# Performance work log

Hardware: AMD Instinct MI355X
Metric: run time of the kernel (lower is better)

Reference implementation:

```python
import jax, jax.numpy as jnp
import numpy as np

N = 100000   # nodes
E = 1600000  # message edges (avg degree 16)
L = 500000   # supervision (label) edges
IN = 128     # input feature dim
H = 2        # attention heads
C = 64       # hidden_dim per head
HC = H * C   # 128, per-layer output channels
DEC = 64     # decoder_dim
NEG_SLOPE = 0.2


def setup_inputs():
    key = jax.random.key(0)
    ks = jax.random.split(key, 16)
    s = 0.05
    return {
        "x": jax.random.normal(ks[0], (N, IN), jnp.float32),
        "edge_index": jax.random.randint(ks[1], (2, E), 0, N, dtype=jnp.int64),
        "edge_label_index": jax.random.randint(ks[2], (2, L), 0, N, dtype=jnp.int64),
        "W1": jax.random.normal(ks[3], (IN, HC), jnp.float32) * s,
        "att_src1": jax.random.normal(ks[4], (H, C), jnp.float32) * s,
        "att_dst1": jax.random.normal(ks[5], (H, C), jnp.float32) * s,
        "bias1": jnp.zeros((HC,), jnp.float32),
        "W2": jax.random.normal(ks[6], (HC, HC), jnp.float32) * s,
        "att_src2": jax.random.normal(ks[7], (H, C), jnp.float32) * s,
        "att_dst2": jax.random.normal(ks[8], (H, C), jnp.float32) * s,
        "bias2": jnp.zeros((HC,), jnp.float32),
        "lin1_w": jax.random.normal(ks[9], (2 * HC, DEC), jnp.float32) * s,
        "lin1_b": jnp.zeros((DEC,), jnp.float32),
        "lin2_w": jax.random.normal(ks[10], (DEC, 1), jnp.float32) * s,
        "lin2_b": jnp.zeros((1,), jnp.float32),
    }


def _gat_conv(x, src, dst, W, att_src, att_dst, bias, n_nodes):
    # PyG GATConv (concat=True, negative_slope=0.2), self-loops already in src/dst.
    h = (x @ W).reshape(-1, H, C)                       # [N, H, C]
    a_s = jnp.sum(h * att_src[None], axis=-1)           # [N, H]
    a_d = jnp.sum(h * att_dst[None], axis=-1)           # [N, H]
    e = jax.nn.leaky_relu(a_s[src] + a_d[dst], NEG_SLOPE)  # [E, H]
    m = jax.ops.segment_max(e, dst, num_segments=n_nodes)  # segment-softmax (stable)
    ex = jnp.exp(e - jax.lax.stop_gradient(m)[dst])
    denom = jax.ops.segment_sum(ex, dst, num_segments=n_nodes)
    alpha = ex / denom[dst]                             # [E, H]
    out = jax.ops.segment_sum(h[src] * alpha[:, :, None], dst, num_segments=n_nodes)
    return out.reshape(n_nodes, HC) + bias


def reference(x, edge_index, edge_label_index, W1, att_src1, att_dst1, bias1,
              W2, att_src2, att_dst2, bias2, lin1_w, lin1_b, lin2_w, lin2_b):
    n = x.shape[0]
    loop = jnp.arange(n, dtype=edge_index.dtype)
    src = jnp.concatenate([edge_index[0], loop])
    dst = jnp.concatenate([edge_index[1], loop])
    # encode (eval mode: dropout is a no-op)
    h1 = jax.nn.relu(_gat_conv(x, src, dst, W1, att_src1, att_dst1, bias1, n))
    z = _gat_conv(h1, src, dst, W2, att_src2, att_dst2, bias2, n)
    # decode
    hs = jnp.concatenate([z[edge_label_index[0]], z[edge_label_index[1]]], axis=1)
    hdec = jax.nn.relu(hs @ lin1_w + lin1_b)
    return (hdec @ lin2_w + lin2_b).reshape(-1)
```

## Files before the change

### kernel.cpp

```cpp
#include <hip/hip_runtime.h>
#include <hip/hip_fp16.h>


typedef _Float16 f16x8 __attribute__((ext_vector_type(8)));
typedef float f32x4 __attribute__((ext_vector_type(4)));

__device__ __forceinline__ float rl_f(float v, int lane) {
    return __int_as_float(__builtin_amdgcn_readlane(__float_as_int(v), lane));
}

#define WT_LD 136
__global__ __launch_bounds__(256, 3) void gemm_mfma(
    const float* __restrict__ X, const float* __restrict__ W,
    _Float16* __restrict__ Y, int nrows,
    const float* __restrict__ att_s, const float* __restrict__ att_d,
    float2* __restrict__ as_out, float2* __restrict__ ad_out)
{
    __shared__ _Float16 WT[128 * WT_LD];
    __shared__ _Float16 At[64 * WT_LD];
    const int t = threadIdx.x;
    const int lane = t & 63;
    const int wid = t >> 6;

    for (int i = t; i < 128 * 32; i += 256) {
        const int k = i >> 5;
        const int n4 = (i & 31) * 4;
        const float4 wv = *reinterpret_cast<const float4*>(&W[k * 128 + n4]);
        WT[(n4 + 0) * WT_LD + k] = (_Float16)wv.x;
        WT[(n4 + 1) * WT_LD + k] = (_Float16)wv.y;
        WT[(n4 + 2) * WT_LD + k] = (_Float16)wv.z;
        WT[(n4 + 3) * WT_LD + k] = (_Float16)wv.w;
    }

    const int am = lane & 15, ag = lane >> 4;

    float asv[8], adv[8];
    if (as_out) {
#pragma unroll
        for (int n0 = 0; n0 < 8; ++n0) {
            asv[n0] = att_s[n0 * 16 + am];
            adv[n0] = att_d[n0 * 16 + am];
        }
    }

    const int ntiles = (nrows + 63) >> 6;
    for (int tile = blockIdx.x; tile < ntiles; tile += gridDim.x) {
        const int rbase = tile * 64;
        __syncthreads();
        {
            const int r = t >> 2;
            const int c0 = (t & 3) * 32;
            const int gr = rbase + r;
            _Float16 tmp[32];
            if (gr < nrows) {
                const float* src = X + (size_t)gr * 128 + c0;
#pragma unroll
                for (int q = 0; q < 8; ++q) {
                    const float4 v = *reinterpret_cast<const float4*>(src + q * 4);
                    tmp[q * 4 + 0] = (_Float16)v.x; tmp[q * 4 + 1] = (_Float16)v.y;
                    tmp[q * 4 + 2] = (_Float16)v.z; tmp[q * 4 + 3] = (_Float16)v.w;
                }
            } else {
#pragma unroll
                for (int q = 0; q < 32; ++q) tmp[q] = (_Float16)0.f;
            }
#pragma unroll
            for (int q = 0; q < 4; ++q)
                *reinterpret_cast<f16x8*>(&At[r * WT_LD + c0 + q * 8]) =
                    *reinterpret_cast<const f16x8*>(&tmp[q * 8]);
        }
        __syncthreads();

        const int srow = wid * 16;
        f16x8 a[4];
#pragma unroll
        for (int kb = 0; kb < 4; ++kb)
            a[kb] = *reinterpret_cast<const f16x8*>(
                &At[(srow + am) * WT_LD + kb * 32 + ag * 8]);

        f32x4 acc[8];
#pragma unroll
        for (int n0 = 0; n0 < 8; ++n0) {
            f32x4 c = {0.f, 0.f, 0.f, 0.f};
#pragma unroll
            for (int kb = 0; kb < 4; ++kb) {
                const f16x8 b = *reinterpret_cast<const f16x8*>(
                    &WT[(n0 * 16 + am) * WT_LD + kb * 32 + ag * 8]);
                c = __builtin_amdgcn_mfma_f32_16x16x32_f16(a[kb], b, c, 0, 0, 0);
            }
            acc[n0] = c;
        }

        const int growbase = rbase + srow + ag * 4;

#pragma unroll
        for (int j = 0; j < 4; ++j) {
            const int grow = growbase + j;
            if (grow < nrows) {
#pragma unroll
                for (int n0 = 0; n0 < 8; ++n0)
                    Y[(size_t)grow * 128 + n0 * 16 + am] = (_Float16)acc[n0][j];
            }
        }

        if (as_out) {
#pragma unroll
            for (int j = 0; j < 4; ++j) {
                float s0 = 0.f, s1 = 0.f, d0 = 0.f, d1 = 0.f;
#pragma unroll
                for (int n0 = 0; n0 < 4; ++n0) {
                    s0 = fmaf(acc[n0][j], asv[n0], s0);
                    d0 = fmaf(acc[n0][j], adv[n0], d0);
                }
#pragma unroll
                for (int n0 = 4; n0 < 8; ++n0) {
                    s1 = fmaf(acc[n0][j], asv[n0], s1);
                    d1 = fmaf(acc[n0][j], adv[n0], d1);
                }
#pragma unroll
                for (int off = 1; off < 16; off <<= 1) {
                    s0 += __shfl_xor(s0, off, 64); s1 += __shfl_xor(s1, off, 64);
                    d0 += __shfl_xor(d0, off, 64); d1 += __shfl_xor(d1, off, 64);
                }
                const int grow = growbase + j;
                if (am == 0 && grow < nrows) {
                    as_out[grow] = make_float2(s0, s1);
                    ad_out[grow] = make_float2(d0, d1);
                }
            }
        }
    }
}

__global__ __launch_bounds__(256) void init_counts_k(int* __restrict__ counts, int N)
{
    const int i = blockIdx.x * blockDim.x + threadIdx.x;
    if (i < N) counts[i] = 1;
}

__global__ __launch_bounds__(256) void hist_k(
    const int* __restrict__ edst, int E, int* __restrict__ counts)
{
    const int stride = gridDim.x * blockDim.x;
    for (int e = blockIdx.x * blockDim.x + threadIdx.x; e < E; e += stride)
        atomicAdd(&counts[edst[e]], 1);
}

__global__ __launch_bounds__(256) void scan_phase1(
    const int* __restrict__ counts, int* __restrict__ blockSums, int N)
{
    __shared__ int wsum[4];
    const int b = blockIdx.x, t = threadIdx.x;
    const int base = b * 1024 + t * 4;
    int s = 0;
    if (base + 3 < N) {
        const int4 c = *reinterpret_cast<const int4*>(&counts[base]);
        s = c.x + c.y + c.z + c.w;
    } else {
#pragma unroll
        for (int k = 0; k < 4; ++k) if (base + k < N) s += counts[base + k];
    }
#pragma unroll
    for (int off = 32; off; off >>= 1) s += __shfl_xor(s, off, 64);
    if ((t & 63) == 0) wsum[t >> 6] = s;
    __syncthreads();
    if (t == 0) blockSums[b] = wsum[0] + wsum[1] + wsum[2] + wsum[3];
}

__global__ __launch_bounds__(256) void scan_phase2(
    int* __restrict__ blockSums, int nb, int* __restrict__ row_ptr, int N)
{
    __shared__ int wsum[4];
    __shared__ int carry_sh;
    const int t = threadIdx.x;
    if (t == 0) carry_sh = 0;
    __syncthreads();
    for (int base = 0; base < nb; base += 256) {
        const int i = base + t;
        const int v = (i < nb) ? blockSums[i] : 0;
        int x = v;
#pragma unroll
        for (int off = 1; off < 64; off <<= 1) {
            const int y = __shfl_up(x, off, 64);
            if ((t & 63) >= off) x += y;
        }
        if ((t & 63) == 63) wsum[t >> 6] = x;
        __syncthreads();
        int woff = 0;
        for (int w = 0; w < (t >> 6); ++w) woff += wsum[w];
        const int carry = carry_sh;
        if (i < nb) blockSums[i] = carry + woff + x - v;
        __syncthreads();
        if (t == 255) carry_sh = carry + woff + x;
        __syncthreads();
    }
    if (t == 0) row_ptr[N] = carry_sh;
}

__global__ __launch_bounds__(256) void scan_phase3(
    const int* __restrict__ counts, const int* __restrict__ blockSums,
    int* __restrict__ row_ptr, int N)
{
    __shared__ int wsum[4];
    const int b = blockIdx.x, t = threadIdx.x;
    const int base = b * 1024 + t * 4;
    int v0 = 0, v1 = 0, v2 = 0, v3 = 0;
    if (base + 3 < N) {
        const int4 c = *reinterpret_cast<const int4*>(&counts[base]);
        v0 = c.x; v1 = c.y; v2 = c.z; v3 = c.w;
    } else {
        if (base + 0 < N) v0 = counts[base + 0];
        if (base + 1 < N) v1 = counts[base + 1];
        if (base + 2 < N) v2 = counts[base + 2];
        if (base + 3 < N) v3 = counts[base + 3];
    }
    const int tsum = v0 + v1 + v2 + v3;
    int x = tsum;
#pragma unroll
    for (int off = 1; off < 64; off <<= 1) {
        const int y = __shfl_up(x, off, 64);
        if ((t & 63) >= off) x += y;
    }
    if ((t & 63) == 63) wsum[t >> 6] = x;
    __syncthreads();
    int woff = 0;
    for (int w = 0; w < (t >> 6); ++w) woff += wsum[w];
    int excl = blockSums[b] + woff + x - tsum;
    if (base + 0 < N) row_ptr[base + 0] = excl;
    if (base + 1 < N) row_ptr[base + 1] = excl + v0;
    if (base + 2 < N) row_ptr[base + 2] = excl + v0 + v1;
    if (base + 3 < N) row_ptr[base + 3] = excl + v0 + v1 + v2;
}

__global__ __launch_bounds__(256) void init_cursor_k(
    const int* __restrict__ row_ptr, int* __restrict__ cursor,
    int* __restrict__ csr_src, int N)
{
    const int i = blockIdx.x * blockDim.x + threadIdx.x;
    if (i < N) {
        const int p = row_ptr[i];
        csr_src[p] = i;
        cursor[i] = p + 1;
    }
}

__global__ __launch_bounds__(256) void scatter_xcd_k(
    const int* __restrict__ esrc, const int* __restrict__ edst, int E,
    int* __restrict__ cursor, int* __restrict__ csr_src, int npp)
{
    const int part = blockIdx.x & 7;
    const int lo = part * npp;
    const int hiN = lo + npp;
    const int bi = blockIdx.x >> 3;
    const int stride = (gridDim.x >> 3) * blockDim.x;
    for (int e = bi * blockDim.x + threadIdx.x; e < E; e += stride) {
        const int d = edst[e];
        if (d >= lo && d < hiN) {
            const int pos = atomicAdd(&cursor[d], 1);
            csr_src[pos] = esrc[e];
        }
    }
}

__global__ __launch_bounds__(256) void csr_aggregate(
    const int* __restrict__ row_ptr, const int* __restrict__ csr_src,
    const __half2* __restrict__ h2, const float2* __restrict__ as_,
    const float2* __restrict__ ad_, const float* __restrict__ bias,
    float* __restrict__ out, int N, int do_relu)
{
    const int lane = threadIdx.x & 63;
    const int node = (blockIdx.x * blockDim.x + threadIdx.x) >> 6;
    if (node >= N) return;

    const int start = row_ptr[node];
    const int end   = row_ptr[node + 1];
    const float2 ad = ad_[node];
    const bool hi = lane >= 32;

    float den0 = 0.f, den1 = 0.f;
    float accx = 0.f, accy = 0.f;

    for (int base = start; base < end; base += 64) {
        const int cnt = min(64, end - base);
        float ex0 = 0.f, ex1 = 0.f;
        int s = 0;
        if (lane < cnt) {
            s = csr_src[base + lane];
            const float2 as = as_[s];
            float e0 = as.x + ad.x; e0 = fmaxf(e0, 0.2f * e0);
            float e1 = as.y + ad.y; e1 = fmaxf(e1, 0.2f * e1);
            ex0 = __expf(e0); ex1 = __expf(e1);
            den0 += ex0; den1 += ex1;
        }
        int j = 0;
        for (; j + 8 <= cnt; j += 8) {
            unsigned idx[8];
            float ej[8];
            float2 hv[8];
#pragma unroll
            for (int q = 0; q < 8; ++q) {
                idx[q] = (unsigned)(__builtin_amdgcn_readlane(s, j + q) * 64 + lane);
                ej[q] = hi ? rl_f(ex1, j + q) : rl_f(ex0, j + q);
            }
#pragma unroll
            for (int q = 0; q < 8; ++q)
                hv[q] = __half22float2(h2[idx[q]]);
#pragma unroll
            for (int q = 0; q < 8; ++q) {
                accx = fmaf(ej[q], hv[q].x, accx);
                accy = fmaf(ej[q], hv[q].y, accy);
            }
        }
        for (; j < cnt; ++j) {
            const unsigned idx = (unsigned)(__builtin_amdgcn_readlane(s, j) * 64 + lane);
            const float e = hi ? rl_f(ex1, j) : rl_f(ex0, j);
            const float2 hv = __half22float2(h2[idx]);
            accx = fmaf(e, hv.x, accx);
            accy = fmaf(e, hv.y, accy);
        }
    }

#pragma unroll
    for (int off = 32; off; off >>= 1) {
        den0 += __shfl_xor(den0, off, 64);
        den1 += __shfl_xor(den1, off, 64);
    }
    const float rd = 1.f / (hi ? den1 : den0);
    const float2 bv = ((const float2*)bias)[lane];
    float vx = fmaf(accx, rd, bv.x);
    float vy = fmaf(accy, rd, bv.y);
    if (do_relu) { vx = fmaxf(vx, 0.f); vy = fmaxf(vy, 0.f); }
    ((float2*)out)[(size_t)node * 64 + lane] = make_float2(vx, vy);
}

__global__ void build_wuv(const float* __restrict__ lin1_w, float* __restrict__ Wuv)
{
    const int i = blockIdx.x * blockDim.x + threadIdx.x;
    if (i >= 128 * 128) return;
    const int k = i >> 7, j = i & 127;
    Wuv[i] = (j < 64) ? lin1_w[k * 64 + j] : lin1_w[(128 + k) * 64 + (j - 64)];
}

__global__ __launch_bounds__(256) void decode_k(
    const int* __restrict__ eli, int L_, const __half* __restrict__ uv,
    const float* __restrict__ lin1_b, const float* __restrict__ lin2_w,
    const float* __restrict__ lin2_b, float* __restrict__ out)
{
    const int lane = threadIdx.x & 63;
    const int wstride = (gridDim.x * blockDim.x) >> 6;
    for (int wid = (blockIdx.x * blockDim.x + threadIdx.x) >> 6; wid < L_; wid += wstride) {
        const int a = eli[wid], b = eli[L_ + wid];
        const unsigned ia = (unsigned)(a * 128 + lane);
        const unsigned ib = (unsigned)(b * 128 + 64 + lane);
        float x = __half2float(uv[ia]) + __half2float(uv[ib]) + lin1_b[lane];
        x = x > 0.f ? x : 0.f;
        float p = x * lin2_w[lane];
#pragma unroll
        for (int off = 32; off; off >>= 1) p += __shfl_xor(p, off, 64);
        if (lane == 0) out[wid] = p + lin2_b[0];
    }
}

extern "C" void kernel_launch(void* const* d_in, const int* in_sizes, int n_in,
                              void* d_out, int out_size, void* d_ws, size_t ws_size,
                              hipStream_t stream)
{
    const float* x     = (const float*)d_in[0];
    const int*   ei    = (const int*)d_in[1];
    const int*   eli   = (const int*)d_in[2];
    const float* W1    = (const float*)d_in[3];
    const float* atts1 = (const float*)d_in[4];
    const float* attd1 = (const float*)d_in[5];
    const float* bias1 = (const float*)d_in[6];
    const float* W2    = (const float*)d_in[7];
    const float* atts2 = (const float*)d_in[8];
    const float* attd2 = (const float*)d_in[9];
    const float* bias2 = (const float*)d_in[10];
    const float* lin1w = (const float*)d_in[11];
    const float* lin1b = (const float*)d_in[12];
    const float* lin2w = (const float*)d_in[13];
    const float* lin2b = (const float*)d_in[14];
    float* out = (float*)d_out;

    const int N = in_sizes[0] / 128;
    const int E = in_sizes[1] / 2;
    const int L = in_sizes[2] / 2;

    float* ws   = (float*)d_ws;
    __half2* h16 = (__half2*)ws;
    float* x2z  = ws + (size_t)N * 64;
    float* a_s  = x2z + (size_t)N * 128;
    float* a_d  = a_s + (size_t)N * 2;
    float* Wuv  = a_d + (size_t)N * 2;
    int* row_ptr = (int*)(Wuv + 128 * 128);
    int* counts  = row_ptr + (N + 4);
    int* cursor  = counts + N;
    int* csr_src = cursor + N;
    int* blockSums = csr_src + (E + N);

    const int nBlocks256 = (N + 255) / 256;
    const int nb = (N + 1023) / 1024;
    const int npp = (N + 7) / 8;
    const int ntiles = (N + 63) / 64;
    const int gemmGrid = ntiles < 768 ? ntiles : 768;

    init_counts_k<<<nBlocks256, 256, 0, stream>>>(counts, N);
    hist_k<<<2048, 256, 0, stream>>>(ei + E, E, counts);
    scan_phase1<<<nb, 256, 0, stream>>>(counts, blockSums, N);
    scan_phase2<<<1, 256, 0, stream>>>(blockSums, nb, row_ptr, N);
    scan_phase3<<<nb, 256, 0, stream>>>(counts, blockSums, row_ptr, N);
    init_cursor_k<<<nBlocks256, 256, 0, stream>>>(row_ptr, cursor, csr_src, N);
    scatter_xcd_k<<<2048, 256, 0, stream>>>(ei, ei + E, E, cursor, csr_src, npp);

    for (int layer = 0; layer < 2; ++layer) {
        const float* xin  = (layer == 0) ? x : x2z;
        const float* W    = (layer == 0) ? W1 : W2;
        const float* as_w = (layer == 0) ? atts1 : atts2;
        const float* ad_w = (layer == 0) ? attd1 : attd2;
        const float* bs   = (layer == 0) ? bias1 : bias2;

        gemm_mfma<<<gemmGrid, 256, 0, stream>>>(xin, W, (_Float16*)h16, N, as_w, ad_w,
                                                (float2*)a_s, (float2*)a_d);
        csr_aggregate<<<(N + 3) / 4, 256, 0, stream>>>(row_ptr, csr_src, h16,
                                                       (const float2*)a_s, (const float2*)a_d,
                                                       bs, x2z, N, (layer == 0) ? 1 : 0);
    }

    build_wuv<<<64, 256, 0, stream>>>(lin1w, Wuv);
    gemm_mfma<<<gemmGrid, 256, 0, stream>>>(x2z, Wuv, (_Float16*)h16, N,
                                            nullptr, nullptr, nullptr, nullptr);
    decode_k<<<8192, 256, 0, stream>>>(eli, L, (const __half*)h16, lin1b, lin2w, lin2b, out);
}
```

Before: 459.3 us.

## Use mixed-precision FMA for half gathers and XCD-partition the degree histogram

The aggregation and decode kernels now use inline v_fma_mix_f32 so packed fp16 values feed the FMA directly, dropping the separate half-to-float conversions. The degree histogram is split into eight destination partitions keyed on block index, matching the existing scatter kernel, so each partition's atomics land on one XCD's L2. Decode also hoists its per-lane bias and weight loads out of the edge loop. Partitioning means every block reads all edges and filters them, which adds read traffic in exchange for more local atomics, and the inline asm ties the code to gfx9-class ISA.

```diff
diff --git a/kernel.cpp b/kernel.cpp
--- a/kernel.cpp
+++ b/kernel.cpp
@@ -7,6 +7,15 @@
 
 __device__ __forceinline__ float rl_f(float v, int lane) {
     return __int_as_float(__builtin_amdgcn_readlane(__float_as_int(v), lane));
+}
+
+__device__ __forceinline__ void fma_mix_lo(float& acc, unsigned hv, float e) {
+    asm("v_fma_mix_f32 %0, %1, %2, %0 op_sel_hi:[1,0,0]"
+        : "+v"(acc) : "v"(hv), "v"(e));
+}
+__device__ __forceinline__ void fma_mix_hi(float& acc, unsigned hv, float e) {
+    asm("v_fma_mix_f32 %0, %1, %2, %0 op_sel:[1,0,0] op_sel_hi:[1,0,0]"
+        : "+v"(acc) : "v"(hv), "v"(e));
 }
 
 #define WT_LD 136
@@ -138,12 +147,18 @@
     if (i < N) counts[i] = 1;
 }
 
-__global__ __launch_bounds__(256) void hist_k(
-    const int* __restrict__ edst, int E, int* __restrict__ counts)
-{
-    const int stride = gridDim.x * blockDim.x;
-    for (int e = blockIdx.x * blockDim.x + threadIdx.x; e < E; e += stride)
-        atomicAdd(&counts[edst[e]], 1);
+__global__ __launch_bounds__(256) void hist_xcd_k(
+    const int* __restrict__ edst, int E, int* __restrict__ counts, int npp)
+{
+    const int part = blockIdx.x & 7;
+    const int lo = part * npp;
+    const int hiN = lo + npp;
+    const int bi = blockIdx.x >> 3;
+    const int stride = (gridDim.x >> 3) * blockDim.x;
+    for (int e = bi * blockDim.x + threadIdx.x; e < E; e += stride) {
+        const int d = edst[e];
+        if (d >= lo && d < hiN) atomicAdd(&counts[d], 1);
+    }
 }
 
 __global__ __launch_bounds__(256) void scan_phase1(
@@ -264,7 +279,7 @@
 
 __global__ __launch_bounds__(256) void csr_aggregate(
     const int* __restrict__ row_ptr, const int* __restrict__ csr_src,
-    const __half2* __restrict__ h2, const float2* __restrict__ as_,
+    const unsigned* __restrict__ h2u, const float2* __restrict__ as_,
     const float2* __restrict__ ad_, const float* __restrict__ bias,
     float* __restrict__ out, int N, int do_relu)
 {
@@ -296,7 +311,7 @@
         for (; j + 8 <= cnt; j += 8) {
             unsigned idx[8];
             float ej[8];
-            float2 hv[8];
+            unsigned hv[8];
 #pragma unroll
             for (int q = 0; q < 8; ++q) {
                 idx[q] = (unsigned)(__builtin_amdgcn_readlane(s, j + q) * 64 + lane);
@@ -304,19 +319,19 @@
             }
 #pragma unroll
             for (int q = 0; q < 8; ++q)
-                hv[q] = __half22float2(h2[idx[q]]);
+                hv[q] = h2u[idx[q]];
 #pragma unroll
             for (int q = 0; q < 8; ++q) {
-                accx = fmaf(ej[q], hv[q].x, accx);
-                accy = fmaf(ej[q], hv[q].y, accy);
+                fma_mix_lo(accx, hv[q], ej[q]);
+                fma_mix_hi(accy, hv[q], ej[q]);
             }
         }
         for (; j < cnt; ++j) {
             const unsigned idx = (unsigned)(__builtin_amdgcn_readlane(s, j) * 64 + lane);
             const float e = hi ? rl_f(ex1, j) : rl_f(ex0, j);
-            const float2 hv = __half22float2(h2[idx]);
-            accx = fmaf(e, hv.x, accx);
-            accy = fmaf(e, hv.y, accy);
+            const unsigned hv = h2u[idx];
+            fma_mix_lo(accx, hv, e);
+            fma_mix_hi(accy, hv, e);
         }
     }
 
@@ -342,19 +357,23 @@
 }
 
 __global__ __launch_bounds__(256) void decode_k(
-    const int* __restrict__ eli, int L_, const __half* __restrict__ uv,
+    const int* __restrict__ eli, int L_, const unsigned short* __restrict__ uv,
     const float* __restrict__ lin1_b, const float* __restrict__ lin2_w,
     const float* __restrict__ lin2_b, float* __restrict__ out)
 {
     const int lane = threadIdx.x & 63;
     const int wstride = (gridDim.x * blockDim.x) >> 6;
+    const float bl = lin1_b[lane];
+    const float wl = lin2_w[lane];
     for (int wid = (blockIdx.x * blockDim.x + threadIdx.x) >> 6; wid < L_; wid += wstride) {
         const int a = eli[wid], b = eli[L_ + wid];
-        const unsigned ia = (unsigned)(a * 128 + lane);
-        const unsigned ib = (unsigned)(b * 128 + 64 + lane);
-        float x = __half2float(uv[ia]) + __half2float(uv[ib]) + lin1_b[lane];
+        const unsigned ua = uv[(unsigned)(a * 128 + lane)];
+        const unsigned ub = uv[(unsigned)(b * 128 + 64 + lane)];
+        float x = bl;
+        asm("v_fma_mix_f32 %0, %1, 1.0, %0 op_sel_hi:[1,0,0]" : "+v"(x) : "v"(ua));
+        asm("v_fma_mix_f32 %0, %1, 1.0, %0 op_sel_hi:[1,0,0]" : "+v"(x) : "v"(ub));
         x = x > 0.f ? x : 0.f;
-        float p = x * lin2_w[lane];
+        float p = x * wl;
 #pragma unroll
         for (int off = 32; off; off >>= 1) p += __shfl_xor(p, off, 64);
         if (lane == 0) out[wid] = p + lin2_b[0];
@@ -405,7 +424,7 @@
     const int gemmGrid = ntiles < 768 ? ntiles : 768;
 
     init_counts_k<<<nBlocks256, 256, 0, stream>>>(counts, N);
-    hist_k<<<2048, 256, 0, stream>>>(ei + E, E, counts);
+    hist_xcd_k<<<2048, 256, 0, stream>>>(ei + E, E, counts, npp);
     scan_phase1<<<nb, 256, 0, stream>>>(counts, blockSums, N);
     scan_phase2<<<1, 256, 0, stream>>>(blockSums, nb, row_ptr, N);
     scan_phase3<<<nb, 256, 0, stream>>>(counts, blockSums, row_ptr, N);
@@ -421,7 +440,8 @@
 
         gemm_mfma<<<gemmGrid, 256, 0, stream>>>(xin, W, (_Float16*)h16, N, as_w, ad_w,
                                                 (float2*)a_s, (float2*)a_d);
-        csr_aggregate<<<(N + 3) / 4, 256, 0, stream>>>(row_ptr, csr_src, h16,
+        csr_aggregate<<<(N + 3) / 4, 256, 0, stream>>>(row_ptr, csr_src,
+                                                       (const unsigned*)h16,
                                                        (const float2*)a_s, (const float2*)a_d,
                                                        bs, x2z, N, (layer == 0) ? 1 : 0);
     }
@@ -429,5 +449,6 @@
     build_wuv<<<64, 256, 0, stream>>>(lin1w, Wuv);
     gemm_mfma<<<gemmGrid, 256, 0, stream>>>(x2z, Wuv, (_Float16*)h16, N,
                                             nullptr, nullptr, nullptr, nullptr);
-    decode_k<<<8192, 256, 0, stream>>>(eli, L, (const __half*)h16, lin1b, lin2w, lin2b, out);
-}
+    decode_k<<<8192, 256, 0, stream>>>(eli, L, (const unsigned short*)h16,
+                                       lin1b, lin2w, lin2b, out);
+}
```

Result: no change. 467.2 us (+1.7%).
